# Performance work log

Measured on AMD Instinct MI355X. Metric: run time of the kernel, lower is better.

## Reference

```python
import jax, jax.numpy as jnp
import numpy as np

N, C, H = 8192, 512, 8


def setup_inputs() -> dict:
    key = jax.random.key(0)
    ks = jax.random.split(key, 5)
    s = 1.0 / np.sqrt(C)
    return {
        "x": jax.random.normal(ks[0], (N, C), dtype=jnp.float32),
        "W_theta": jax.random.normal(ks[1], (C, C), dtype=jnp.float32) * s,
        "b_theta": jnp.zeros((C,), dtype=jnp.float32),
        "W_phi": jax.random.normal(ks[2], (C, C), dtype=jnp.float32) * s,
        "b_phi": jnp.zeros((C,), dtype=jnp.float32),
        "W_k": jax.random.normal(ks[3], (H, C, C), dtype=jnp.float32) * s,
        "b_k": jnp.zeros((H, C), dtype=jnp.float32),
    }


def reference(x, W_theta, b_theta, W_phi, b_phi, W_k, b_k):
    # query/key projections: (N, C)
    query = x @ W_theta + b_theta
    key = x @ W_phi + b_phi
    # dense N x N similarity + row softmax
    sim = query @ key.T                       # (N, N)
    adj = jax.nn.softmax(sim, axis=-1)        # (N, N)
    # per-head V projections, batched: (H, N, C)
    xk = jnp.einsum("nc,hcd->hnd", x, W_k) + b_k[:, None, :]
    # attention-weighted aggregation per head, relu, mean over heads
    out = jnp.einsum("nm,hmd->hnd", adj, xk)  # (H, N, C)
    return jax.nn.relu(out).mean(axis=0)      # (N, C)
```

## Files before the change

### kernel.cpp

```cpp
#include <hip/hip_runtime.h>
#include <hip/hip_bf16.h>
#include <cstdint>
#include <cstddef>

#define NN 8192
#define CC 512
#define HH 8

typedef __attribute__((ext_vector_type(8))) short short8;
typedef __attribute__((ext_vector_type(4))) float f32x4;

__device__ __forceinline__ void gload_lds16(const void* g, void* l) {
  __builtin_amdgcn_global_load_lds(
      (const __attribute__((address_space(1))) void*)g,
      (__attribute__((address_space(3))) void*)l, 16, 0, 0);
}

__device__ __forceinline__ f32x4 mfma16(short8 a, short8 b, f32x4 c) {
  return __builtin_amdgcn_mfma_f32_16x16x32_bf16(a, b, c, 0, 0, 0);
}

__device__ __forceinline__ float b2f(unsigned u) {
  union { unsigned i; float f; } x; x.i = u << 16; return x.f;
}

__device__ __forceinline__ void unpack8(uint4 v, float* f) {
  f[0] = b2f(v.x & 0xffffu); f[1] = b2f(v.x >> 16);
  f[2] = b2f(v.y & 0xffffu); f[3] = b2f(v.y >> 16);
  f[4] = b2f(v.z & 0xffffu); f[5] = b2f(v.z >> 16);
  f[6] = b2f(v.w & 0xffffu); f[7] = b2f(v.w >> 16);
}

__global__ __launch_bounds__(256, 2) void gemm_qk(
    const __hip_bfloat16* __restrict__ ah, const __hip_bfloat16* __restrict__ al, int lda,
    const __hip_bfloat16* __restrict__ bh, const __hip_bfloat16* __restrict__ bl, int ldb,
    int K,
    __hip_bfloat16* __restrict__ outHi, __hip_bfloat16* __restrict__ outLo, int ldc,
    const float* __restrict__ biasCol)
{
  __shared__ __align__(16) char lds[32768];
  const int tid  = threadIdx.x;
  const int lane = tid & 63;
  const int wave = tid >> 6;
  const int bm = blockIdx.y, bn = blockIdx.x;
  const int wr = wave >> 1, wc = wave & 1;
  const int fr = lane & 15, fq = lane >> 4;

  f32x4 acc[4][4] = {};

  for (int kt = 0; kt < K; kt += 32) {
    __syncthreads();
#pragma unroll
    for (int tile = 0; tile < 4; ++tile) {
      const __hip_bfloat16* tp = (tile == 0) ? ah : (tile == 1) ? al
                               : (tile == 2) ? bh : bl;
      const int ld = (tile < 2) ? lda : ldb;
      const int tb = ((tile < 2) ? bm : bn) * 128;
#pragma unroll
      for (int half = 0; half < 2; ++half) {
        int sub = half * 256 + tid;
        int row = sub >> 2, ch = sub & 3;
        gload_lds16(tp + (size_t)(tb + row) * ld + kt + ch * 8,
                    lds + tile * 8192 + sub * 16);
      }
    }
    __syncthreads();

    short8 fah[4], fal[4], fbh[4], fbl[4];
#pragma unroll
    for (int i = 0; i < 4; ++i) {
      const int ra = (wr * 64 + i * 16 + fr) * 64 + fq * 16;
      const int rb = (wc * 64 + i * 16 + fr) * 64 + fq * 16;
      fah[i] = *(const short8*)(lds +         ra);
      fal[i] = *(const short8*)(lds +  8192 + ra);
      fbh[i] = *(const short8*)(lds + 16384 + rb);
      fbl[i] = *(const short8*)(lds + 24576 + rb);
    }
#pragma unroll
    for (int i = 0; i < 4; ++i)
#pragma unroll
      for (int j = 0; j < 4; ++j) {
        acc[i][j] = mfma16(fah[i], fbh[j], acc[i][j]);
        acc[i][j] = mfma16(fah[i], fbl[j], acc[i][j]);
        acc[i][j] = mfma16(fal[i], fbh[j], acc[i][j]);
      }
  }

#pragma unroll
  for (int i = 0; i < 4; ++i)
#pragma unroll
    for (int j = 0; j < 4; ++j) {
      const int rbase = bm * 128 + wr * 64 + i * 16 + fq * 4;
      const int col   = bn * 128 + wc * 64 + j * 16 + fr;
#pragma unroll
      for (int t = 0; t < 4; ++t) {
        float v = acc[i][j][t] + biasCol[col];
        __hip_bfloat16 h = __float2bfloat16(v);
        outHi[(size_t)(rbase + t) * ldc + col] = h;
        outLo[(size_t)(rbase + t) * ldc + col] = __float2bfloat16(v - __bfloat162float(h));
      }
    }
}

__global__ __launch_bounds__(512, 2) void gemm_sim(
    const __hip_bfloat16* __restrict__ A, int lda,
    const __hip_bfloat16* __restrict__ B, int ldb,
    int K,
    float* __restrict__ segMax, unsigned char* __restrict__ sim4)
{
  (void)K;
  __shared__ __align__(16) char lds[65536];
  const int tid  = threadIdx.x;
  const int lane = tid & 63;
  const int wave = tid >> 6;
  const int bm = blockIdx.y, bn = blockIdx.x;
  const int wm = wave >> 2;
  const int wn = wave & 3;
  const int fr = lane & 15, fq = lane >> 4;

  int s0 = tid * 16;          s0 ^= ((s0 >> 9) & 1) << 5;
  int s1 = 8192 + tid * 16;   s1 ^= ((s1 >> 9) & 1) << 5;
  const int off0 = (s0 >> 6) * 1024 + ((s0 & 63) >> 1);
  const int off1 = (s1 >> 6) * 1024 + ((s1 & 63) >> 1);

  const int fl = ((fr >> 3) & 1) << 5;
  const int baseAs = (((wm * 128 + fr) * 64) + fq * 16) ^ fl;
  const int baseBs = (((wn * 64 + fr) * 64) + fq * 16) ^ fl;

  const __hip_bfloat16* Ab = A + (size_t)bm * 256 * lda;
  const __hip_bfloat16* Bb = B + (size_t)bn * 256 * ldb;

#define STAGE_TILE(t, db) do {                                              \
    const __hip_bfloat16* ap_ = Ab + (t) * 32;                              \
    const __hip_bfloat16* bp_ = Bb + (t) * 32;                              \
    gload_lds16(ap_ + off0, lds + (db) * 16384 + tid * 16);                 \
    gload_lds16(ap_ + off1, lds + (db) * 16384 + 8192 + tid * 16);          \
    gload_lds16(bp_ + off0, lds + 32768 + (db) * 16384 + tid * 16);         \
    gload_lds16(bp_ + off1, lds + 32768 + (db) * 16384 + 8192 + tid * 16);  \
  } while (0)

  f32x4 acc[8][4] = {};

  STAGE_TILE(0, 0);
  STAGE_TILE(1, 1);

#pragma unroll
  for (int t = 0; t < 16; ++t) {
    const int db = t & 1;
    if (t == 15) asm volatile("s_waitcnt vmcnt(0)" ::: "memory");
    else         asm volatile("s_waitcnt vmcnt(4)" ::: "memory");
    __builtin_amdgcn_s_barrier();
    __builtin_amdgcn_sched_barrier(0);

    short8 a[8], b4[4];
#pragma unroll
    for (int i = 0; i < 8; ++i)
      a[i] = *(const short8*)(lds + db * 16384 + baseAs + i * 1024);
#pragma unroll
    for (int j = 0; j < 4; ++j)
      b4[j] = *(const short8*)(lds + 32768 + db * 16384 + baseBs + j * 1024);

    __builtin_amdgcn_s_setprio(1);
#pragma unroll
    for (int i = 0; i < 4; ++i)
#pragma unroll
      for (int j = 0; j < 4; ++j)
        acc[i][j] = mfma16(a[i], b4[j], acc[i][j]);
    __builtin_amdgcn_s_setprio(0);

    asm volatile("s_waitcnt lgkmcnt(0)" ::: "memory");
    __builtin_amdgcn_s_barrier();
    __builtin_amdgcn_sched_barrier(0);

    if (t < 14) STAGE_TILE(t + 2, db);
    __builtin_amdgcn_s_setprio(1);
#pragma unroll
    for (int i = 4; i < 8; ++i)
#pragma unroll
      for (int j = 0; j < 4; ++j)
        acc[i][j] = mfma16(a[i], b4[j], acc[i][j]);
    __builtin_amdgcn_s_setprio(0);
    __builtin_amdgcn_s_barrier();
  }
#undef STAGE_TILE

  const int seg = bn * 4 + wn;
#pragma unroll
  for (int i = 0; i < 8; ++i)
#pragma unroll
    for (int tt = 0; tt < 4; ++tt) {
      const int row = bm * 256 + wm * 128 + i * 16 + fq * 4 + tt;
      float mx = fmaxf(fmaxf(acc[i][0][tt], acc[i][1][tt]),
                       fmaxf(acc[i][2][tt], acc[i][3][tt]));
      mx = fmaxf(mx, __shfl_xor(mx, 1));
      mx = fmaxf(mx, __shfl_xor(mx, 2));
      mx = fmaxf(mx, __shfl_xor(mx, 4));
      mx = fmaxf(mx, __shfl_xor(mx, 8));
      if (fr == 0) segMax[(size_t)row * 128 + seg] = mx;
      unsigned q[4];
#pragma unroll
      for (int j = 0; j < 4; ++j)
        q[j] = (unsigned)fminf((mx - acc[i][j][tt]) * (4.0f / 3.0f), 15.0f);
      unsigned char* dst = sim4 + (size_t)row * (NN / 2) + seg * 32 + fr;
      dst[0]  = (unsigned char)(q[0] | (q[1] << 4));
      dst[16] = (unsigned char)(q[2] | (q[3] << 4));
    }
}

__global__ __launch_bounds__(256) void select_zgather(
    const float* __restrict__ segMax, const unsigned char* __restrict__ sim4,
    const __hip_bfloat16* __restrict__ QKhi, const __hip_bfloat16* __restrict__ QKlo,
    const float* __restrict__ x,
    __hip_bfloat16* __restrict__ z)
{
  const int lane = threadIdx.x & 63;
  const int n = blockIdx.x * 4 + (threadIdx.x >> 6);

  float2 sm = ((const float2*)(segMax + (size_t)n * 128))[lane];
  float M = fmaxf(sm.x, sm.y);
#pragma unroll
  for (int off = 32; off; off >>= 1) M = fmaxf(M, __shfl_xor(M, off));

  const unsigned long long b0 = __ballot(sm.x > M - 11.0f);
  const unsigned long long b1 = __ballot(sm.y > M - 11.0f);

  float qf[8];
  {
    uint4 qh4 = ((const uint4*)(QKhi + (size_t)n * 1024))[lane];
    uint4 ql4 = ((const uint4*)(QKlo + (size_t)n * 1024))[lane];
    float a[8], b[8];
    unpack8(qh4, a); unpack8(ql4, b);
#pragma unroll
    for (int e = 0; e < 8; ++e) qf[e] = a[e] + b[e];
  }

  const unsigned char* srow4 = sim4 + (size_t)n * (NN / 2);
  const int jj = lane >> 4;
  const int shift = (jj & 1) * 4;
  const int boff = (jj >> 1) * 16 + (lane & 15);

  int nk = 0;
  float se_mine = -1e30f;
  int   mm_mine = 0;
#pragma unroll
  for (int half = 0; half < 2; ++half) {
    unsigned long long mask = half ? b1 : b0;
    while (mask) {
      const int b = __ffsll((unsigned long long)mask) - 1;
      mask &= mask - 1;
      const int seg = 2 * b + half;
      const float segv = __shfl(half ? sm.y : sm.x, b);
      const unsigned byte = srow4[seg * 32 + boff];
      const float sa = segv - 0.75f * (float)((byte >> shift) & 15u);
      unsigned long long cm = __ballot(sa > M - 11.0f);
      while (cm) {
        const int c = __ffsll((unsigned long long)cm) - 1;
        cm &= cm - 1;
        const int m = seg * 64 + c;
        uint4 kh4 = ((const uint4*)(QKhi + (size_t)m * 1024 + 512))[lane];
        uint4 kl4 = ((const uint4*)(QKlo + (size_t)m * 1024 + 512))[lane];
        float a[8], bb[8];
        unpack8(kh4, a); unpack8(kl4, bb);
        float p = 0.f;
#pragma unroll
        for (int e = 0; e < 8; ++e) p += qf[e] * (a[e] + bb[e]);
#pragma unroll
        for (int off = 32; off; off >>= 1) p += __shfl_xor(p, off);
        if (p > M - 10.5f) {
          if (lane == nk) { se_mine = p; mm_mine = m; }
          nk = (nk < 63) ? nk + 1 : nk;
        }
      }
    }
  }

  float Me = (lane < nk) ? se_mine : -1e30f;
#pragma unroll
  for (int off = 32; off; off >>= 1) Me = fmaxf(Me, __shfl_xor(Me, off));
  const float wv = __expf(se_mine - Me);
  float Lr = (lane < nk) ? wv : 0.f;
#pragma unroll
  for (int off = 32; off; off >>= 1) Lr += __shfl_xor(Lr, off);

  float acc[8] = {};
  for (int i = 0; i < nk; ++i) {
    const int   m = __shfl(mm_mine, i);
    const float w = __shfl(wv, i);
    const float4* row = (const float4*)(x + (size_t)m * CC + 8 * lane);
    float4 a = row[0], b = row[1];
    acc[0] += w * a.x; acc[1] += w * a.y; acc[2] += w * a.z; acc[3] += w * a.w;
    acc[4] += w * b.x; acc[5] += w * b.y; acc[6] += w * b.z; acc[7] += w * b.w;
  }
  const float inv = 1.0f / Lr;
  short8 o;
#pragma unroll
  for (int e = 0; e < 8; ++e) {
    __hip_bfloat16 h = __float2bfloat16(acc[e] * inv);
    o[e] = *(short*)&h;
  }
  *(short8*)(z + (size_t)n * CC + 8 * lane) = o;
}

__global__ __launch_bounds__(256, 2) void gemm_zwk(
    const __hip_bfloat16* __restrict__ z,
    const __hip_bfloat16* __restrict__ WkT,
    const float* __restrict__ bk,
    float* __restrict__ out)
{
  __shared__ __align__(16) char lds[16384];
  const int tid  = threadIdx.x;
  const int lane = tid & 63;
  const int wave = tid >> 6;
  const int bn = blockIdx.x, bm = blockIdx.y, hg = blockIdx.z;
  const int wr = wave >> 1, wc = wave & 1;
  const int fr = lane & 15, fq = lane >> 4;

  f32x4 oacc[4][4] = {};

  for (int hh = 0; hh < 4; ++hh) {
    const int head = hg * 4 + hh;
    const __hip_bfloat16* B = WkT + (size_t)(head * 512 + bn * 128) * CC;
    f32x4 acc[4][4] = {};
    for (int kt = 0; kt < CC; kt += 32) {
      __syncthreads();
#pragma unroll
      for (int half = 0; half < 2; ++half) {
        int sub = half * 256 + tid;
        int row = sub >> 2, ch = sub & 3;
        gload_lds16(z + (size_t)(bm * 128 + row) * CC + kt + ch * 8, lds +        sub * 16);
        gload_lds16(B + (size_t)row * CC + kt + ch * 8,              lds + 8192 + sub * 16);
      }
      __syncthreads();

      short8 af[4], bf[4];
#pragma unroll
      for (int i = 0; i < 4; ++i) {
        af[i] = *(const short8*)(lds +        (wr * 64 + i * 16 + fr) * 64 + fq * 16);
        bf[i] = *(const short8*)(lds + 8192 + (wc * 64 + i * 16 + fr) * 64 + fq * 16);
      }
#pragma unroll
      for (int i = 0; i < 4; ++i)
#pragma unroll
        for (int j = 0; j < 4; ++j)
          acc[i][j] = mfma16(af[i], bf[j], acc[i][j]);
    }
#pragma unroll
    for (int j = 0; j < 4; ++j) {
      const int d = bn * 128 + wc * 64 + j * 16 + fr;
      const float bias = bk[head * CC + d];
#pragma unroll
      for (int i = 0; i < 4; ++i)
#pragma unroll
        for (int t = 0; t < 4; ++t)
          oacc[i][j][t] += fmaxf(acc[i][j][t] + bias, 0.f);
    }
  }

#pragma unroll
  for (int i = 0; i < 4; ++i)
#pragma unroll
    for (int j = 0; j < 4; ++j) {
      const int rbase = bm * 128 + wr * 64 + i * 16 + fq * 4;
      const int d     = bn * 128 + wc * 64 + j * 16 + fr;
#pragma unroll
      for (int t = 0; t < 4; ++t)
        atomicAdd(out + (size_t)(rbase + t) * CC + d, 0.125f * oacc[i][j][t]);
    }
}

__global__ void prep_all(const float* __restrict__ x,
                         const float* __restrict__ Wth, const float* __restrict__ Wph,
                         const float* __restrict__ bt, const float* __restrict__ bp,
                         const float* __restrict__ Wk,
                         __hip_bfloat16* __restrict__ xhi, __hip_bfloat16* __restrict__ xlo,
                         __hip_bfloat16* __restrict__ wthi, __hip_bfloat16* __restrict__ wtlo,
                         __hip_bfloat16* __restrict__ wkt, float* __restrict__ biasqk,
                         float* __restrict__ outz) {
  int idx = blockIdx.x * 256 + threadIdx.x;
  if (idx < 4194304) {
    float v = x[idx];
    __hip_bfloat16 h = __float2bfloat16(v);
    xhi[idx] = h;
    xlo[idx] = __float2bfloat16(v - __bfloat162float(h));
  } else if (idx < 4718592) {
    int i = idx - 4194304;
    int j = i >> 9, c = i & 511;
    const float* W = (j < 512) ? Wth : Wph;
    float v = W[(size_t)c * 512 + (j & 511)];
    __hip_bfloat16 h = __float2bfloat16(v);
    wthi[i] = h;
    wtlo[i] = __float2bfloat16(v - __bfloat162float(h));
  } else if (idx < 6815744) {
    int i = idx - 4718592;
    int j = i >> 9, c = i & 511;
    float v = Wk[(size_t)(j >> 9) * 262144 + (size_t)c * 512 + (j & 511)];
    wkt[i] = __float2bfloat16(v);
  } else if (idx < 6816768) {
    int i = idx - 6815744;
    biasqk[i] = (i < 512) ? bt[i] : bp[i - 512];
  } else if (idx < 7865344) {
    int i = idx - 6816768;
    ((float4*)outz)[i] = make_float4(0.f, 0.f, 0.f, 0.f);
  }
}

extern "C" void kernel_launch(void* const* d_in, const int* in_sizes, int n_in,
                              void* d_out, int out_size, void* d_ws, size_t ws_size,
                              hipStream_t stream) {
  const float* x  = (const float*)d_in[0];
  const float* Wt = (const float*)d_in[1];
  const float* bt = (const float*)d_in[2];
  const float* Wp = (const float*)d_in[3];
  const float* bp = (const float*)d_in[4];
  const float* Wk = (const float*)d_in[5];
  const float* bk = (const float*)d_in[6];
  float* out = (float*)d_out;

  const size_t MB = 1024 * 1024;
  char* w = (char*)d_ws;
  __hip_bfloat16* xhi  = (__hip_bfloat16*)(w + 0 * MB);
  __hip_bfloat16* xlo  = (__hip_bfloat16*)(w + 8 * MB);
  __hip_bfloat16* WThi = (__hip_bfloat16*)(w + 16 * MB);
  __hip_bfloat16* WTlo = (__hip_bfloat16*)(w + 17 * MB);
  float*          biasqk = (float*)(w + 18 * MB);
  __hip_bfloat16* WkT  = (__hip_bfloat16*)(w + 20 * MB);
  __hip_bfloat16* QKhi = (__hip_bfloat16*)(w + 24 * MB);
  __hip_bfloat16* QKlo = (__hip_bfloat16*)(w + 40 * MB);
  __hip_bfloat16* z    = (__hip_bfloat16*)(w + 56 * MB);
  float*          segMax = (float*)(w + 64 * MB);
  unsigned char*  sim4   = (unsigned char*)(w + 68 * MB);

  prep_all<<<7865344 / 256, 256, 0, stream>>>(x, Wt, Wp, bt, bp, Wk,
                                              xhi, xlo, WThi, WTlo, WkT, biasqk,
                                              out);

  gemm_qk<<<dim3(1024 / 128, NN / 128), 256, 0, stream>>>(
      xhi, xlo, CC, WThi, WTlo, CC, CC, QKhi, QKlo, 1024, biasqk);

  gemm_sim<<<dim3(NN / 256, NN / 256), 512, 0, stream>>>(
      QKhi, 1024, QKhi + 512, 1024, CC, segMax, sim4);

  select_zgather<<<NN / 4, 256, 0, stream>>>(segMax, sim4, QKhi, QKlo, x, z);

  gemm_zwk<<<dim3(CC / 128, NN / 128, 2), 256, 0, stream>>>(z, WkT, bk, out);
}
```

Measured before the change: 324.0 us.

## Triple-buffer LDS in similarity GEMM and drop per-iteration barriers

Switches the sim GEMM main loop from double to triple LDS buffering (96KB), which allows the two mid-iteration barriers to be removed. Global-to-LDS staging for tile t+2 is split into two halves, and each half is issued between the LDS fragment reads and the MFMA groups. The aim is to cut synchronisation stalls and overlap loads with compute. The larger LDS footprint may stop the two blocks per CU that launch_bounds asks for from fitting, which would lower occupancy.

```diff
diff --git a/kernel.cpp b/kernel.cpp
--- a/kernel.cpp
+++ b/kernel.cpp
@@ -109,7 +109,7 @@
     float* __restrict__ segMax, unsigned char* __restrict__ sim4)
 {
   (void)K;
-  __shared__ __align__(16) char lds[65536];
+  __shared__ __align__(16) char lds[98304];
   const int tid  = threadIdx.x;
   const int lane = tid & 63;
   const int wave = tid >> 6;
@@ -130,36 +130,47 @@
   const __hip_bfloat16* Ab = A + (size_t)bm * 256 * lda;
   const __hip_bfloat16* Bb = B + (size_t)bn * 256 * ldb;
 
-#define STAGE_TILE(t, db) do {                                              \
-    const __hip_bfloat16* ap_ = Ab + (t) * 32;                              \
-    const __hip_bfloat16* bp_ = Bb + (t) * 32;                              \
-    gload_lds16(ap_ + off0, lds + (db) * 16384 + tid * 16);                 \
-    gload_lds16(ap_ + off1, lds + (db) * 16384 + 8192 + tid * 16);          \
-    gload_lds16(bp_ + off0, lds + 32768 + (db) * 16384 + tid * 16);         \
-    gload_lds16(bp_ + off1, lds + 32768 + (db) * 16384 + 8192 + tid * 16);  \
+#define STAGE_C0(t, buf) do {                                                \
+    const __hip_bfloat16* ap_ = Ab + (t) * 32;                               \
+    const __hip_bfloat16* bp_ = Bb + (t) * 32;                               \
+    gload_lds16(ap_ + off0, lds + (buf) * 16384 + tid * 16);                 \
+    gload_lds16(bp_ + off0, lds + 49152 + (buf) * 16384 + tid * 16);         \
   } while (0)
+#define STAGE_C1(t, buf) do {                                                \
+    const __hip_bfloat16* ap_ = Ab + (t) * 32;                               \
+    const __hip_bfloat16* bp_ = Bb + (t) * 32;                               \
+    gload_lds16(ap_ + off1, lds + (buf) * 16384 + 8192 + tid * 16);          \
+    gload_lds16(bp_ + off1, lds + 49152 + (buf) * 16384 + 8192 + tid * 16);  \
+  } while (0)
 
   f32x4 acc[8][4] = {};
 
-  STAGE_TILE(0, 0);
-  STAGE_TILE(1, 1);
+  STAGE_C0(0, 0); STAGE_C1(0, 0);
+  STAGE_C0(1, 1); STAGE_C1(1, 1);
 
 #pragma unroll
   for (int t = 0; t < 16; ++t) {
-    const int db = t & 1;
+    const int buf = t % 3;
+    const int nbuf = (t + 2) % 3;
+    const char* Abuf = lds + buf * 16384;
+    const char* Bbuf = lds + 49152 + buf * 16384;
+
     if (t == 15) asm volatile("s_waitcnt vmcnt(0)" ::: "memory");
     else         asm volatile("s_waitcnt vmcnt(4)" ::: "memory");
     __builtin_amdgcn_s_barrier();
     __builtin_amdgcn_sched_barrier(0);
 
-    short8 a[8], b4[4];
-#pragma unroll
-    for (int i = 0; i < 8; ++i)
-      a[i] = *(const short8*)(lds + db * 16384 + baseAs + i * 1024);
+    short8 a[4], b4[4];
+#pragma unroll
+    for (int i = 0; i < 4; ++i)
+      a[i] = *(const short8*)(Abuf + baseAs + i * 1024);
 #pragma unroll
     for (int j = 0; j < 4; ++j)
-      b4[j] = *(const short8*)(lds + 32768 + db * 16384 + baseBs + j * 1024);
-
+      b4[j] = *(const short8*)(Bbuf + baseBs + j * 1024);
+    if (t < 14) STAGE_C0(t + 2, nbuf);
+
+    asm volatile("s_waitcnt lgkmcnt(0)" ::: "memory");
+    __builtin_amdgcn_sched_barrier(0);
     __builtin_amdgcn_s_setprio(1);
 #pragma unroll
     for (int i = 0; i < 4; ++i)
@@ -168,21 +179,24 @@
         acc[i][j] = mfma16(a[i], b4[j], acc[i][j]);
     __builtin_amdgcn_s_setprio(0);
 
+    short8 a2[4];
+#pragma unroll
+    for (int i = 0; i < 4; ++i)
+      a2[i] = *(const short8*)(Abuf + baseAs + (4 + i) * 1024);
+    if (t < 14) STAGE_C1(t + 2, nbuf);
+
     asm volatile("s_waitcnt lgkmcnt(0)" ::: "memory");
-    __builtin_amdgcn_s_barrier();
     __builtin_amdgcn_sched_barrier(0);
-
-    if (t < 14) STAGE_TILE(t + 2, db);
     __builtin_amdgcn_s_setprio(1);
 #pragma unroll
-    for (int i = 4; i < 8; ++i)
+    for (int i = 0; i < 4; ++i)
 #pragma unroll
       for (int j = 0; j < 4; ++j)
-        acc[i][j] = mfma16(a[i], b4[j], acc[i][j]);
+        acc[4 + i][j] = mfma16(a2[i], b4[j], acc[4 + i][j]);
     __builtin_amdgcn_s_setprio(0);
-    __builtin_amdgcn_s_barrier();
-  }
-#undef STAGE_TILE
+  }
+#undef STAGE_C0
+#undef STAGE_C1
 
   const int seg = bn * 4 + wn;
 #pragma unroll
```

New measurement: 342.8 us. 1.06x slower.
